# Kernel optimization log

Measured on AMD Instinct MI355X. Metric: run time of the kernel, lower is better.

## Reference

```python
import jax, jax.numpy as jnp
import numpy as np

N, E, IN, H, OUT = 50000, 600000, 256, 128, 40
EPS, GAMMA = 0.1, 0.1  # PyG AntiSymmetricConv defaults


def _build_norm(edge_index, n):
    # GCNConv normalization with added self loops: D^-1/2 (A+I) D^-1/2
    loops = jnp.arange(n, dtype=edge_index.dtype)
    src = jnp.concatenate([edge_index[0], loops])
    dst = jnp.concatenate([edge_index[1], loops])
    deg = jax.ops.segment_sum(jnp.ones(src.shape[0], dtype=jnp.float32), dst, num_segments=n)
    dinv = jnp.where(deg > 0, jax.lax.rsqrt(jnp.maximum(deg, 1e-12)), 0.0)
    return src, dst, dinv[src] * dinv[dst]


def _gcn(x, w, src, dst, norm, n):
    # GCNConv(bias=False): scatter normalized messages to target nodes
    m = (x @ w)[src] * norm[:, None]          # [E+N, d]
    return jax.ops.segment_sum(m, dst, num_segments=n)


def _antisym_conv(x, W, gcn_w, bias, src, dst, norm, num_iters):
    d = W.shape[0]
    aW = W - W.T - GAMMA * jnp.eye(d, dtype=W.dtype)  # antisymmetric weight
    n = x.shape[0]

    def step(h, _):
        upd = jnp.tanh(h @ aW.T + _gcn(h, gcn_w, src, dst, norm, n) + bias)
        return h + EPS * upd, None

    x, _ = jax.lax.scan(step, x, None, length=num_iters)
    return x


def setup_inputs() -> dict:
    key = jax.random.key(0)
    ks = jax.random.split(key, 16)
    s = lambda fan: 1.0 / np.sqrt(fan)
    return {
        "x": jax.random.normal(ks[0], (N, IN), dtype=jnp.float32),
        "edge_index": jax.random.randint(ks[1], (2, E), 0, N, dtype=jnp.int64),
        "w_hid": jax.random.normal(ks[2], (H, IN), dtype=jnp.float32) * s(IN),
        "b_hid": jax.random.normal(ks[3], (H,), dtype=jnp.float32) * s(IN),
        "W_a1": jax.random.normal(ks[4], (H, H), dtype=jnp.float32) * s(H),
        "gcn_w1": jax.random.normal(ks[5], (H, H), dtype=jnp.float32) * s(H),
        "b_a1": jax.random.normal(ks[6], (H,), dtype=jnp.float32) * s(H),
        "w_hid2": jax.random.normal(ks[7], (H // 2, H), dtype=jnp.float32) * s(H),
        "b_hid2": jax.random.normal(ks[8], (H // 2,), dtype=jnp.float32) * s(H),
        "W_a2": jax.random.normal(ks[9], (H // 2, H // 2), dtype=jnp.float32) * s(H // 2),
        "gcn_w2": jax.random.normal(ks[10], (H // 2, H // 2), dtype=jnp.float32) * s(H // 2),
        "b_a2": jax.random.normal(ks[11], (H // 2,), dtype=jnp.float32) * s(H // 2),
        "w_fc": jax.random.normal(ks[12], (OUT, H // 2), dtype=jnp.float32) * s(H // 2),
        "b_fc": jax.random.normal(ks[13], (OUT,), dtype=jnp.float32) * s(H // 2),
    }


def reference(x, edge_index, w_hid, b_hid, W_a1, gcn_w1, b_a1,
              w_hid2, b_hid2, W_a2, gcn_w2, b_a2, w_fc, b_fc):
    n = x.shape[0]
    src, dst, norm = _build_norm(edge_index, n)
    h = jax.nn.leaky_relu(x @ w_hid.T + b_hid)          # dropout is no-op in eval
    h = _antisym_conv(h, W_a1, gcn_w1, b_a1, src, dst, norm, num_iters=3)
    h = jax.nn.leaky_relu(h)
    h = jax.nn.leaky_relu(h @ w_hid2.T + b_hid2)
    h = _antisym_conv(h, W_a2, gcn_w2, b_a2, src, dst, norm, num_iters=1)
    out = h @ w_fc.T + b_fc
    return jax.nn.log_softmax(out, axis=1)
```

## Files before the change

### kernel.cpp

```cpp
#include <hip/hip_runtime.h>
#include <hip/hip_bf16.h>
#include <math.h>

typedef unsigned short u16;
typedef unsigned int   u32;
using short8  = __attribute__((ext_vector_type(8))) short;
using f32x4   = __attribute__((ext_vector_type(4))) float;

static constexpr int NNODE = 50000;
static constexpr int NEDGE = 600000;
static constexpr float EPSC   = 0.1f;
static constexpr float GAMMAC = 0.1f;

static constexpr int NTILE = (NNODE + 63) / 64;
static constexpr int GH    = 128;
static constexpr int NRNG  = 12500;
static constexpr int NWORD = NRNG / 2;
static constexpr int NPASS = 4;

static constexpr long long O_DINV   = 0;
static constexpr long long O_DEGI   = 50000;
static constexpr long long O_ROWPTR = 100000;
static constexpr long long O_GCUR   = 150004;
static constexpr long long O_ECSR   = 200260;
static constexpr long long O_WHB    = 1400260;
static constexpr long long O_G1TB   = O_WHB  + 16384;
static constexpr long long O_AW1B   = O_G1TB + 8192;
static constexpr long long O_W2B    = O_AW1B + 8192;
static constexpr long long O_AW2B   = O_W2B  + 4096;
static constexpr long long O_G2TB   = O_AW2B + 2048;
static constexpr long long O_WFCB   = O_G2TB + 2048;
static constexpr long long O_AGGB   = 3450004;
static constexpr long long O_HB0    = O_AGGB + 3200000;
static constexpr long long O_HB1    = O_HB0  + 3200000;
static constexpr long long O_S0     = O_HB1  + 3200000;
static constexpr long long O_S1     = O_S0   + 1600000;
static constexpr long long O_PART   = O_S1   + 1600000;
static constexpr long long O_BASE   = O_PART + 3200000;

__device__ __forceinline__ float bf2f(u16 u) {
    return __uint_as_float(((unsigned)u) << 16);
}
__device__ __forceinline__ u16 f2bf(float f) {
    unsigned u = __float_as_uint(f);
    return (u16)((u + 0x7FFFu + ((u >> 16) & 1u)) >> 16);
}
__device__ __forceinline__ float ftanh(float x) {
    float x2 = fminf(fmaxf(2.f * x, -30.f), 30.f);
    float e = __expf(x2);
    return (e - 1.f) * __builtin_amdgcn_rcpf(e + 1.f);
}
__device__ __forceinline__ u16 pk_fp8(float a, float b) {
    int pk = __builtin_amdgcn_cvt_pk_fp8_f32(a, b, 0, false);
    return (u16)(pk & 0xffff);
}
__device__ __forceinline__ void acc_fp8x4(float* a, u32 v, float w) {
    a[0] += __builtin_amdgcn_cvt_f32_fp8(v, 0) * w;
    a[1] += __builtin_amdgcn_cvt_f32_fp8(v, 1) * w;
    a[2] += __builtin_amdgcn_cvt_f32_fp8(v, 2) * w;
    a[3] += __builtin_amdgcn_cvt_f32_fp8(v, 3) * w;
}

__global__ __launch_bounds__(256) void prep_kernel(
    const float* __restrict__ w_hid, const float* __restrict__ W_a1,
    const float* __restrict__ gcn1,  const float* __restrict__ w2,
    const float* __restrict__ W_a2,  const float* __restrict__ gcn2,
    const float* __restrict__ wfc,   float* __restrict__ ws)
{
    int j = blockIdx.x * 256 + threadIdx.x;
    if (j < 32768) { ((u16*)(ws+O_WHB))[j] = f2bf(w_hid[j]); return; } j -= 32768;
    if (j < 16384) { int r=j>>7, c=j&127; ((u16*)(ws+O_G1TB))[j] = f2bf(gcn1[c*128+r]); return; } j -= 16384;
    if (j < 16384) { int r=j>>7, c=j&127;
                     ((u16*)(ws+O_AW1B))[j] = f2bf(W_a1[r*128+c] - W_a1[c*128+r] - (r==c?GAMMAC:0.f));
                     return; } j -= 16384;
    if (j < 8192)  { ((u16*)(ws+O_W2B))[j] = f2bf(w2[j]); return; } j -= 8192;
    if (j < 4096)  { int r=j>>6, c=j&63;
                     ((u16*)(ws+O_AW2B))[j] = f2bf(W_a2[r*64+c] - W_a2[c*64+r] - (r==c?GAMMAC:0.f));
                     return; } j -= 4096;
    if (j < 4096)  { int r=j>>6, c=j&63; ((u16*)(ws+O_G2TB))[j] = f2bf(gcn2[c*64+r]); return; } j -= 4096;
    if (j < 2560)  { ((u16*)(ws+O_WFCB))[j] = f2bf(wfc[j]); return; } j -= 2560;
    if (j == 0)    { ((int*)(ws+O_GCUR))[0] = 0; }
}

__global__ __launch_bounds__(256) void alloc_kernel(
    const u16* __restrict__ part, float* __restrict__ dinv,
    int* __restrict__ degi, int* __restrict__ rowptr,
    u16* __restrict__ base16, int* __restrict__ gcur)
{
    int i = blockIdx.x * 256 + threadIdx.x;
    int lane = threadIdx.x & 63;
    bool ok = i < NNODE;
    int deg = 0;
    if (ok) {
        int run = 0;
        #pragma unroll 4
        for (int g = 0; g < GH; ++g) {
            base16[(long long)g * NNODE + i] = (u16)run;
            run += part[(long long)g * NNODE + i];
        }
        deg = run;
        degi[i] = deg;
        dinv[i] = rsqrtf(1.0f + (float)deg);
    }
    int run = deg;
    #pragma unroll
    for (int off = 1; off < 64; off <<= 1) {
        int v = __shfl_up(run, off);
        if (lane >= off) run += v;
    }
    int tot = __shfl(run, 63);
    int basep = 0;
    if (lane == 63) basep = atomicAdd(gcur, tot);
    basep = __shfl(basep, 63);
    if (ok) rowptr[i] = basep + run - deg;
}

__global__ __launch_bounds__(256) void fill_kernel(
    const int* __restrict__ ei, const float* __restrict__ dinv,
    const int* __restrict__ rowptr, const u16* __restrict__ base16,
    int2* __restrict__ ecsr)
{
    __shared__ u32 cur[NWORD];
    const int g    = blockIdx.x >> 2;
    const int pass = blockIdx.x & 3;
    const long long e0 = (long long)g * NEDGE / GH;
    const long long e1 = (long long)(g + 1) * NEDGE / GH;
    const u16* bb = base16 + (long long)g * NNODE;
    const int nbase = pass * NRNG;
    for (int wi = threadIdx.x; wi < NWORD; wi += 256) cur[wi] = 0;
    __syncthreads();
    for (long long e = e0 + threadIdx.x; e < e1; e += 256) {
        int d = ei[NEDGE + e];
        int r = d - nbase;
        if ((unsigned)r < (unsigned)NRNG) {
            int s = ei[e];
            u32 old = atomicAdd(&cur[r >> 1], 1u << ((r & 1) * 16));
            int rank = (int)((old >> ((r & 1) * 16)) & 0xffffu);
            int slot = rowptr[d] + (int)bb[d] + rank;
            int2 v;
            v.x = s;
            v.y = __float_as_int(dinv[s]);
            ecsr[slot] = v;
        }
    }
}

template<int KS, int NT, int AF32, int LOADACT, int EPI>
__global__ __launch_bounds__(256, 4) void mgemm(
    const void* __restrict__ Araw,
    const u16* __restrict__ Bt,
    const float* __restrict__ bias,
    float* __restrict__ outF,
    u16* __restrict__ outB,
    u16* __restrict__ outB8,
    int M, int Nn, int ldc,
    const int* __restrict__ ei,
    u16* __restrict__ partial)
{
    constexpr int K    = KS * 32;
    constexpr int KCHU = (K > 128) ? 128 : K;
    constexpr int KC   = KCHU / 32;
    constexpr int NCH  = K / KCHU;
    constexpr int P    = KCHU + 8;
    constexpr int ROWS = NT * 16;
    constexpr int CW   = NT * 16 + 1;
    constexpr int BSZ  = ROWS * P * 2;
    constexpr int ASZ  = 64 * CW * 4;
    constexpr int SMEM = BSZ > ASZ ? BSZ : ASZ;
    __shared__ __align__(16) char smem[SMEM];

    if (ei && blockIdx.x >= NTILE) {
        int g = blockIdx.x - NTILE;
        u32* hist = (u32*)smem;
        const long long e0 = (long long)g * NEDGE / GH;
        const long long e1 = (long long)(g + 1) * NEDGE / GH;
        u16* part = partial + (long long)g * NNODE;
        for (int pass = 0; pass < NPASS; ++pass) {
            const int nbase = pass * NRNG;
            for (int wi = threadIdx.x; wi < NWORD; wi += 256) hist[wi] = 0;
            __syncthreads();
            for (long long e = e0 + threadIdx.x; e < e1; e += 256) {
                int d = ei[NEDGE + e];
                int r = d - nbase;
                if ((unsigned)r < (unsigned)NRNG)
                    atomicAdd(&hist[r >> 1], 1u << ((r & 1) * 16));
            }
            __syncthreads();
            for (int wi = threadIdx.x; wi < NWORD; wi += 256)
                *(u32*)&part[nbase + wi * 2] = hist[wi];
            __syncthreads();
        }
        return;
    }

    u16*   bl   = (u16*)smem;
    float* accL = (float*)smem;

    const int wave = threadIdx.x >> 6;
    const int lane = threadIdx.x & 63;
    const int m = lane & 15, q = lane >> 4;
    const int rowbase = blockIdx.x * 64 + wave * 16;
    const int row = rowbase + m;
    const bool rok = row < M;
    const short8 z8 = {0,0,0,0,0,0,0,0};

    short8 af[KS];
    if (AF32) {
        const float* apf = (const float*)Araw + (long long)row * K;
        #pragma unroll
        for (int k = 0; k < KS; ++k) {
            short8 t = z8;
            if (rok) {
                const float4* p = (const float4*)(apf + (k * 4 + q) * 8);
                float4 a = p[0], b = p[1];
                t[0]=(short)f2bf(a.x); t[1]=(short)f2bf(a.y); t[2]=(short)f2bf(a.z); t[3]=(short)f2bf(a.w);
                t[4]=(short)f2bf(b.x); t[5]=(short)f2bf(b.y); t[6]=(short)f2bf(b.z); t[7]=(short)f2bf(b.w);
            }
            af[k] = t;
        }
    } else {
        const short8* ap = (const short8*)((const u16*)Araw + (long long)row * K);
        #pragma unroll
        for (int k = 0; k < KS; ++k) af[k] = rok ? ap[k * 4 + q] : z8;
    }
    if (LOADACT) {
        #pragma unroll
        for (int k = 0; k < KS; ++k)
            #pragma unroll
            for (int e = 0; e < 8; ++e) {
                float f = bf2f((u16)af[k][e]);
                f = f > 0.f ? f : 0.01f * f;
                af[k][e] = (short)f2bf(f);
            }
    }

    f32x4 acc[NT];
    #pragma unroll
    for (int j = 0; j < NT; ++j) acc[j] = (f32x4){0.f,0.f,0.f,0.f};

    for (int ch = 0; ch < NCH; ++ch) {
        if (ch) __syncthreads();
        constexpr int CHUNKS = ROWS * (KCHU / 8);
        for (int t = threadIdx.x; t < CHUNKS; t += 256) {
            int r = t / (KCHU / 8), c = t - r * (KCHU / 8);
            short8 v = z8;
            if (r < Nn) v = *(const short8*)&Bt[(long long)r * K + ch * KCHU + c * 8];
            *(short8*)&bl[r * P + c * 8] = v;
        }
        __syncthreads();
        #pragma unroll
        for (int j = 0; j < NT; ++j) {
            #pragma unroll
            for (int k = 0; k < KC; ++k) {
                short8 bf_ = *(const short8*)&bl[(j * 16 + m) * P + k * 32 + q * 8];
                acc[j] = __builtin_amdgcn_mfma_f32_16x16x32_bf16(af[ch * KC + k], bf_, acc[j], 0, 0, 0);
            }
        }
    }

    __syncthreads();
    #pragma unroll
    for (int j = 0; j < NT; ++j)
        #pragma unroll
        for (int r = 0; r < 4; ++r)
            accL[(wave * 16 + q * 4 + r) * CW + j * 16 + m] = acc[j][r];
    __syncthreads();

    const int c0 = lane * 2;
    if (c0 < NT * 16) {
        float2 bv = {0.f, 0.f};
        if (bias) {
            if (c0 < Nn)     bv.x = bias[c0];
            if (c0 + 1 < Nn) bv.y = bias[c0 + 1];
        }
        #pragma unroll
        for (int rl = 0; rl < 16; ++rl) {
            int rowD = rowbase + rl;
            if (rowD >= M) continue;
            float2 v = *(const float2*)&accL[(wave * 16 + rl) * CW + c0];
            long long o = (long long)rowD * ldc + c0;
            v.x += bv.x; v.y += bv.y;
            if (EPI == 1) {
                v.x = v.x > 0.f ? v.x : 0.01f * v.x;
                v.y = v.y > 0.f ? v.y : 0.01f * v.y;
            }
            if (c0 + 1 < Nn) {
                if (outB) { ushort2 ob; ob.x = f2bf(v.x); ob.y = f2bf(v.y);
                            *(ushort2*)&outB[o] = ob; }
                if (outB8) outB8[o >> 1] = pk_fp8(v.x, v.y);
                if (outF) { *(float2*)&outF[o] = v; }
            } else if (c0 < Nn) {
                if (outB) outB[o] = f2bf(v.x);
                if (outF) outF[o] = v.x;
            }
        }
    }
}

template<int HD>
__global__ __launch_bounds__(256) void gather_kernel(
    const int* __restrict__ rowptr, const int* __restrict__ degi,
    const int2* __restrict__ ecsr, const float* __restrict__ dinv,
    const u32* __restrict__ g8, u16* __restrict__ aggB)
{
    int node = (blockIdx.x * 256 + threadIdx.x) >> 6;
    int lane = threadIdx.x & 63;
    if (node >= NNODE) return;
    const int qr = lane >> 4, l4 = lane & 15;
    const int r0 = rowptr[node];
    const int r1 = r0 + degi[node];
    const float dn = dinv[node];
    constexpr int EL = (HD == 128) ? 8 : 4;

    float a[EL];
    #pragma unroll
    for (int i = 0; i < EL; ++i) a[i] = 0.f;
    if (qr == 0) {
        if (HD == 128) {
            uint2 gv = ((const uint2*)g8)[(long long)node * 16 + l4];
            acc_fp8x4(a, gv.x, dn);
            acc_fp8x4(a + 4, gv.y, dn);
        } else {
            u32 gv = g8[(long long)node * 16 + l4];
            acc_fp8x4(a, gv, dn);
        }
    }

    for (int base = r0; base < r1; base += 64) {
        int idx = base + lane;
        int cs = 0; float cw = 0.f;
        if (idx < r1) { int2 ev = ecsr[idx]; cs = ev.x; cw = __int_as_float(ev.y); }
        int cnt = min(64, r1 - base);
        for (int j = 0; j < cnt; j += 16) {
            #pragma unroll
            for (int u = 0; u < 4; ++u) {
                int jj = j + u * 4 + qr;
                int   s = __shfl(cs, jj);
                float w = __shfl(cw, jj);
                if (HD == 128) {
                    uint2 gv = ((const uint2*)g8)[(long long)s * 16 + l4];
                    acc_fp8x4(a, gv.x, w);
                    acc_fp8x4(a + 4, gv.y, w);
                } else {
                    u32 gv = g8[(long long)s * 16 + l4];
                    acc_fp8x4(a, gv, w);
                }
            }
        }
    }

    #pragma unroll
    for (int i = 0; i < EL; ++i) {
        a[i] += __shfl_xor(a[i], 16);
        a[i] += __shfl_xor(a[i], 32);
    }
    if (HD == 128) {
        float v0 = (qr == 0) ? a[0] : (qr == 1) ? a[2] : (qr == 2) ? a[4] : a[6];
        float v1 = (qr == 0) ? a[1] : (qr == 1) ? a[3] : (qr == 2) ? a[5] : a[7];
        v0 *= dn; v1 *= dn;
        long long o = (long long)node * 128 + l4 * 8 + qr * 2;
        ushort2 ob; ob.x = f2bf(v0); ob.y = f2bf(v1);
        *(ushort2*)&aggB[o] = ob;
    } else {
        float v = (qr == 0) ? a[0] : (qr == 1) ? a[1] : (qr == 2) ? a[2] : a[3];
        aggB[(long long)node * 64 + l4 * 4 + qr] = f2bf(v * dn);
    }
}

template<int KS, int NT, int TAIL>
__global__ __launch_bounds__(256, TAIL ? 3 : 4) void mgemm_conv(
    const u16* __restrict__ hA,
    const u16* __restrict__ gA,
    const u16* __restrict__ BtW,
    const u16* __restrict__ BtG,
    const float* __restrict__ bias,
    u16* __restrict__ outB,
    u16* __restrict__ outB8,
    const u16* __restrict__ w2W,
    const float* __restrict__ b2,
    int M)
{
    constexpr int K    = KS * 32;
    constexpr int Nn   = NT * 16;
    constexpr int P    = K + 8;
    constexpr int CW   = Nn + 1;
    constexpr int BSZ  = Nn * P * 2;
    constexpr int ASZ  = 64 * CW * 4;
    constexpr int R1   = BSZ > ASZ ? BSZ : ASZ;
    constexpr int EXTRA = TAIL ? 64 * P * 2 : 0;
    __shared__ __align__(16) char smem[R1 + EXTRA];
    u16*   bl   = (u16*)smem;
    float* accL = (float*)smem;
    u16*   aggT = (u16*)(smem + R1);

    const int wave = threadIdx.x >> 6;
    const int lane = threadIdx.x & 63;
    const int m = lane & 15, q = lane >> 4;
    const int rowbase = blockIdx.x * 64 + wave * 16;
    const int row = rowbase + m;
    const bool rok = row < M;
    const short8 z8 = {0,0,0,0,0,0,0,0};

    short8 af1[KS], af2[KS];
    {
        const short8* ap1 = (const short8*)(hA + (long long)row * K);
        const short8* ap2 = (const short8*)(gA + (long long)row * K);
        #pragma unroll
        for (int k = 0; k < KS; ++k) {
            af1[k] = rok ? ap1[k * 4 + q] : z8;
            af2[k] = rok ? ap2[k * 4 + q] : z8;
        }
    }

    f32x4 acc[NT];
    #pragma unroll
    for (int j = 0; j < NT; ++j) acc[j] = (f32x4){0.f,0.f,0.f,0.f};

    #pragma unroll
    for (int pass = 0; pass < 2; ++pass) {
        const u16* Bcur = pass ? BtG : BtW;
        if (pass) __syncthreads();
        constexpr int CHUNKS = Nn * (K / 8);
        for (int t = threadIdx.x; t < CHUNKS; t += 256) {
            int r = t / (K / 8), c = t - r * (K / 8);
            *(short8*)&bl[r * P + c * 8] = *(const short8*)&Bcur[(long long)r * K + c * 8];
        }
        __syncthreads();
        #pragma unroll
        for (int j = 0; j < NT; ++j) {
            #pragma unroll
            for (int k = 0; k < KS; ++k) {
                short8 bf_ = *(const short8*)&bl[(j * 16 + m) * P + k * 32 + q * 8];
                acc[j] = __builtin_amdgcn_mfma_f32_16x16x32_bf16(
                    pass ? af2[k] : af1[k], bf_, acc[j], 0, 0, 0);
            }
        }
    }

    __syncthreads();
    #pragma unroll
    for (int j = 0; j < NT; ++j)
        #pragma unroll
        for (int r = 0; r < 4; ++r)
            accL[(wave * 16 + q * 4 + r) * CW + j * 16 + m] = acc[j][r];
    __syncthreads();

    const int c0 = lane * 2;
    if (TAIL == 0) {
        if (c0 < Nn) {
            float2 bv = {bias[c0], bias[c0 + 1]};
            #pragma unroll
            for (int rl = 0; rl < 16; ++rl) {
                int rowD = rowbase + rl;
                if (rowD >= M) continue;
                float2 v = *(const float2*)&accL[(wave * 16 + rl) * CW + c0];
                long long o = (long long)rowD * Nn + c0;
                ushort2 hh = *(const ushort2*)&hA[o];
                float n0 = bf2f(hh.x) + EPSC * ftanh(v.x + bv.x);
                float n1 = bf2f(hh.y) + EPSC * ftanh(v.y + bv.y);
                ushort2 ob; ob.x = f2bf(n0); ob.y = f2bf(n1);
                *(ushort2*)&outB[o] = ob;
                if (outB8) outB8[o >> 1] = pk_fp8(n0, n1);
            }
        }
        return;
    }

    {
        float2 bv = {bias[c0], bias[c0 + 1]};
        #pragma unroll
        for (int rl = 0; rl < 16; ++rl) {
            int rowD = rowbase + rl;
            float n0 = 0.f, n1 = 0.f;
            if (rowD < M) {
                float2 v = *(const float2*)&accL[(wave * 16 + rl) * CW + c0];
                long long o = (long long)rowD * K + c0;
                ushort2 hh = *(const ushort2*)&hA[o];
                n0 = bf2f(hh.x) + EPSC * ftanh(v.x + bv.x);
                n1 = bf2f(hh.y) + EPSC * ftanh(v.y + bv.y);
                n0 = n0 > 0.f ? n0 : 0.01f * n0;
                n1 = n1 > 0.f ? n1 : 0.01f * n1;
            }
            ushort2 ob; ob.x = f2bf(n0); ob.y = f2bf(n1);
            *(ushort2*)&aggT[(wave * 16 + rl) * P + c0] = ob;
        }
    }
    __syncthreads();

    short8 af3[4];
    #pragma unroll
    for (int k = 0; k < 4; ++k)
        af3[k] = *(const short8*)&aggT[(wave * 16 + m) * P + k * 32 + q * 8];

    {
        constexpr int CH2 = 64 * 16;
        for (int t = threadIdx.x; t < CH2; t += 256) {
            int r = t >> 4, c = t & 15;
            *(short8*)&bl[r * P + c * 8] = *(const short8*)&w2W[(long long)r * K + c * 8];
        }
    }
    __syncthreads();

    f32x4 acc2[4];
    #pragma unroll
    for (int j = 0; j < 4; ++j) acc2[j] = (f32x4){0.f,0.f,0.f,0.f};
    #pragma unroll
    for (int j = 0; j < 4; ++j)
        #pragma unroll
        for (int k = 0; k < 4; ++k) {
            short8 bf_ = *(const short8*)&bl[(j * 16 + m) * P + k * 32 + q * 8];
            acc2[j] = __builtin_amdgcn_mfma_f32_16x16x32_bf16(af3[k], bf_, acc2[j], 0, 0, 0);
        }

    __syncthreads();
    constexpr int CW2 = 65;
    #pragma unroll
    for (int j = 0; j < 4; ++j)
        #pragma unroll
        for (int r = 0; r < 4; ++r)
            accL[(wave * 16 + q * 4 + r) * CW2 + j * 16 + m] = acc2[j][r];
    __syncthreads();

    if (c0 < 64) {
        float2 bv = {b2[c0], b2[c0 + 1]};
        #pragma unroll
        for (int rl = 0; rl < 16; ++rl) {
            int rowD = rowbase + rl;
            if (rowD >= M) continue;
            float2 v = *(const float2*)&accL[(wave * 16 + rl) * CW2 + c0];
            v.x += bv.x; v.y += bv.y;
            v.x = v.x > 0.f ? v.x : 0.01f * v.x;
            v.y = v.y > 0.f ? v.y : 0.01f * v.y;
            long long o = (long long)rowD * 64 + c0;
            ushort2 ob; ob.x = f2bf(v.x); ob.y = f2bf(v.y);
            *(ushort2*)&outB[o] = ob;
            outB8[o >> 1] = pk_fp8(v.x, v.y);
        }
    }
}

__global__ __launch_bounds__(256, 4) void conv2fc(
    const u16* __restrict__ hA,
    const u16* __restrict__ gA,
    const u16* __restrict__ BtW, const u16* __restrict__ BtG,
    const float* __restrict__ bias,
    const u16* __restrict__ wfcB, const float* __restrict__ bfc,
    float* __restrict__ outF, int M)
{
    constexpr int K  = 64, NT = 4, KS = 2;
    constexpr int P  = K + 8;
    constexpr int CW = 65;
    constexpr int R1 = 64 * CW * 4;
    __shared__ __align__(16) char smem[R1 + 64 * P * 2];
    u16*   bl   = (u16*)smem;
    float* accL = (float*)smem;
    u16*   aggT = (u16*)(smem + R1);

    const int wave = threadIdx.x >> 6;
    const int lane = threadIdx.x & 63;
    const int m = lane & 15, q = lane >> 4;
    const int rowbase = blockIdx.x * 64 + wave * 16;
    const int row = rowbase + m;
    const bool rok = row < M;
    const short8 z8 = {0,0,0,0,0,0,0,0};

    short8 af1[KS], af2[KS];
    {
        const short8* ap1 = (const short8*)(hA + (long long)row * K);
        const short8* ap2 = (const short8*)(gA + (long long)row * K);
        #pragma unroll
        for (int k = 0; k < KS; ++k) {
            af1[k] = rok ? ap1[k * 4 + q] : z8;
            af2[k] = rok ? ap2[k * 4 + q] : z8;
        }
    }

    f32x4 acc[NT];
    #pragma unroll
    for (int j = 0; j < NT; ++j) acc[j] = (f32x4){0.f,0.f,0.f,0.f};

    #pragma unroll
    for (int pass = 0; pass < 2; ++pass) {
        const u16* Bcur = pass ? BtG : BtW;
        if (pass) __syncthreads();
        constexpr int CHUNKS = 64 * (K / 8);
        for (int t = threadIdx.x; t < CHUNKS; t += 256) {
            int r = t >> 3, c = t & 7;
            *(short8*)&bl[r * P + c * 8] = *(const short8*)&Bcur[(long long)r * K + c * 8];
        }
        __syncthreads();
        #pragma unroll
        for (int j = 0; j < NT; ++j)
            #pragma unroll
            for (int k = 0; k < KS; ++k) {
                short8 bf_ = *(const short8*)&bl[(j * 16 + m) * P + k * 32 + q * 8];
                acc[j] = __builtin_amdgcn_mfma_f32_16x16x32_bf16(
                    pass ? af2[k] : af1[k], bf_, acc[j], 0, 0, 0);
            }
    }

    __syncthreads();
    #pragma unroll
    for (int j = 0; j < NT; ++j)
        #pragma unroll
        for (int r = 0; r < 4; ++r)
            accL[(wave * 16 + q * 4 + r) * CW + j * 16 + m] = acc[j][r];
    __syncthreads();

    {
        const int c0 = lane * 2;
        float2 bv = {bias[c0 & 63], bias[(c0 + 1) & 63]};
        if (c0 < 64) {
            #pragma unroll
            for (int rl = 0; rl < 16; ++rl) {
                int rowD = rowbase + rl;
                float n0 = 0.f, n1 = 0.f;
                if (rowD < M) {
                    float2 v = *(const float2*)&accL[(wave * 16 + rl) * CW + c0];
                    long long o = (long long)rowD * 64 + c0;
                    ushort2 hh = *(const ushort2*)&hA[o];
                    n0 = bf2f(hh.x) + EPSC * ftanh(v.x + bv.x);
                    n1 = bf2f(hh.y) + EPSC * ftanh(v.y + bv.y);
                }
                ushort2 ob; ob.x = f2bf(n0); ob.y = f2bf(n1);
                *(ushort2*)&aggT[(wave * 16 + rl) * P + c0] = ob;
            }
        }
    }
    __syncthreads();

    short8 af4[KS];
    #pragma unroll
    for (int k = 0; k < KS; ++k)
        af4[k] = *(const short8*)&aggT[(wave * 16 + m) * P + k * 32 + q * 8];

    {
        constexpr int CHF = 48 * 8;
        for (int t = threadIdx.x; t < CHF; t += 256) {
            int r = t >> 3, c = t & 7;
            short8 v = z8;
            if (r < 40) v = *(const short8*)&wfcB[(long long)r * K + c * 8];
            *(short8*)&bl[r * P + c * 8] = v;
        }
    }
    __syncthreads();

    f32x4 acc3[3];
    #pragma unroll
    for (int j = 0; j < 3; ++j) acc3[j] = (f32x4){0.f,0.f,0.f,0.f};
    #pragma unroll
    for (int j = 0; j < 3; ++j)
        #pragma unroll
        for (int k = 0; k < KS; ++k) {
            short8 bf_ = *(const short8*)&bl[(j * 16 + m) * P + k * 32 + q * 8];
            acc3[j] = __builtin_amdgcn_mfma_f32_16x16x32_bf16(af4[k], bf_, acc3[j], 0, 0, 0);
        }

    __syncthreads();
    constexpr int CW3 = 49;
    #pragma unroll
    for (int j = 0; j < 3; ++j)
        #pragma unroll
        for (int r = 0; r < 4; ++r)
            accL[(wave * 16 + q * 4 + r) * CW3 + j * 16 + m] = acc3[j][r];
    __syncthreads();

    float mrow = 0.f, lrow = 0.f;
    if (lane < 16) {
        const float* rp = &accL[(wave * 16 + lane) * CW3];
        float mx = -1e30f;
        for (int c = 0; c < 40; ++c) mx = fmaxf(mx, rp[c] + bfc[c]);
        float s = 0.f;
        for (int c = 0; c < 40; ++c) s += expf(rp[c] + bfc[c] - mx);
        mrow = mx; lrow = logf(s);
    }
    for (int rl = 0; rl < 16; ++rl) {
        float mm = __shfl(mrow, rl);
        float ll = __shfl(lrow, rl);
        int rowD = rowbase + rl;
        if (rowD < M && lane < 40) {
            float v = accL[(wave * 16 + rl) * CW3 + lane] + bfc[lane];
            outF[(long long)rowD * 40 + lane] = v - mm - ll;
        }
    }
}

extern "C" void kernel_launch(void* const* d_in, const int* in_sizes, int n_in,
                              void* d_out, int out_size, void* d_ws, size_t ws_size,
                              hipStream_t stream) {
    const float* x     = (const float*)d_in[0];
    const int*   ei    = (const int*)d_in[1];
    const float* w_hid = (const float*)d_in[2];
    const float* b_hid = (const float*)d_in[3];
    const float* W_a1  = (const float*)d_in[4];
    const float* gcn1  = (const float*)d_in[5];
    const float* b_a1  = (const float*)d_in[6];
    const float* w2    = (const float*)d_in[7];
    const float* b2    = (const float*)d_in[8];
    const float* W_a2  = (const float*)d_in[9];
    const float* gcn2  = (const float*)d_in[10];
    const float* b_a2  = (const float*)d_in[11];
    const float* wfc   = (const float*)d_in[12];
    const float* bfc   = (const float*)d_in[13];
    float* ws = (float*)d_ws;
    float* out = (float*)d_out;

    float* dinv   = ws + O_DINV;
    int*   degi   = (int*)(ws + O_DEGI);
    int*   rowptr = (int*)(ws + O_ROWPTR);
    int*   gcur   = (int*)(ws + O_GCUR);
    int2*  ecsr   = (int2*)(ws + O_ECSR);
    u16* whB  = (u16*)(ws + O_WHB);
    u16* g1tB = (u16*)(ws + O_G1TB);
    u16* aw1B = (u16*)(ws + O_AW1B);
    u16* w2B  = (u16*)(ws + O_W2B);
    u16* aw2B = (u16*)(ws + O_AW2B);
    u16* g2tB = (u16*)(ws + O_G2TB);
    u16* wfcB = (u16*)(ws + O_WFCB);
    u16* aggB = (u16*)(ws + O_AGGB);
    u16* hB0  = (u16*)(ws + O_HB0);
    u16* hB1  = (u16*)(ws + O_HB1);
    u16* s0   = (u16*)(ws + O_S0);
    u16* s1   = (u16*)(ws + O_S1);
    u16* part = (u16*)(ws + O_PART);
    u16* base16 = (u16*)(ws + O_BASE);

    prep_kernel<<<(84481 + 255) / 256, 256, 0, stream>>>(
        w_hid, W_a1, gcn1, w2, W_a2, gcn2, wfc, ws);

    const int gatherBlocks = (NNODE * 64 + 255) / 256;

    mgemm<8, 8, 1, 0, 1><<<NTILE + GH, 256, 0, stream>>>(
        x, whB, b_hid, nullptr, hB0, s0, NNODE, 128, 128, ei, part);

    alloc_kernel<<<(NNODE + 255) / 256, 256, 0, stream>>>(
        part, dinv, degi, rowptr, base16, gcur);
    fill_kernel<<<GH * NPASS, 256, 0, stream>>>(ei, dinv, rowptr, base16, ecsr);

    gather_kernel<128><<<gatherBlocks, 256, 0, stream>>>(
        rowptr, degi, ecsr, dinv, (const u32*)s0, aggB);
    mgemm_conv<4, 8, 0><<<NTILE, 256, 0, stream>>>(
        hB0, aggB, aw1B, g1tB, b_a1, hB1, s1, nullptr, nullptr, NNODE);
    gather_kernel<128><<<gatherBlocks, 256, 0, stream>>>(
        rowptr, degi, ecsr, dinv, (const u32*)s1, aggB);
    mgemm_conv<4, 8, 0><<<NTILE, 256, 0, stream>>>(
        hB1, aggB, aw1B, g1tB, b_a1, hB0, s0, nullptr, nullptr, NNODE);
    gather_kernel<128><<<gatherBlocks, 256, 0, stream>>>(
        rowptr, degi, ecsr, dinv, (const u32*)s0, aggB);
    mgemm_conv<4, 8, 1><<<NTILE, 256, 0, stream>>>(
        hB0, aggB, aw1B, g1tB, b_a1, hB1, s1, w2B, b2, NNODE);

    gather_kernel<64><<<gatherBlocks, 256, 0, stream>>>(
        rowptr, degi, ecsr, dinv, (const u32*)s1, aggB);
    conv2fc<<<NTILE, 256, 0, stream>>>(
        hB1, aggB, aw2B, g2tB, b_a2, wfcB, bfc, out, NNODE);
}
```

Before: 362.9 us.

## Fuse first-iteration gather into conv GEMM and shrink tail conv shared memory

Adds an fconv kernel, 512 threads per block, that gathers the fp8 neighbour features for 64 nodes into shared memory and then runs both conv GEMMs and the tanh update in the same block. It replaces the first gather_kernel plus mgemm_conv pair, so the aggregated tensor no longer makes a round trip through global memory and one launch is removed. The tail variant of mgemm_conv now reuses its main shared buffer for the aggregate tile and the second weight, staging values in registers across a barrier so it can run with launch bounds of 4 instead of 3. The risk is that the gather phase in fconv uses fewer, larger blocks, which may give less latency hiding than the standalone gather.

New measurement: 355.9 us. No clear change (-1.9%).

```diff
diff --git a/kernel.cpp b/kernel.cpp
--- a/kernel.cpp
+++ b/kernel.cpp
@@ -367,8 +367,136 @@
     }
 }
 
+__global__ __launch_bounds__(512, 3) void fconv(
+    const u16* __restrict__ hA, const u32* __restrict__ g8,
+    const int* __restrict__ rowptr, const int* __restrict__ degi,
+    const int2* __restrict__ ecsr, const float* __restrict__ dinv,
+    const u16* __restrict__ BtW, const u16* __restrict__ BtG,
+    const float* __restrict__ bias,
+    u16* __restrict__ outB, u16* __restrict__ outB8)
+{
+    constexpr int K = 128, P = 136;
+    __shared__ __align__(16) char smem[52224];
+    u16* bl   = (u16*)smem;
+    u16* aggT = (u16*)(smem + 34816);
+    const int wave = threadIdx.x >> 6, lane = threadIdx.x & 63;
+    const int m = lane & 15, q = lane >> 4;
+    const int blockrow = blockIdx.x * 64;
+    const short8 z8 = {0,0,0,0,0,0,0,0};
+
+    {
+        const int qr = q, l4 = m;
+        for (int nn = 0; nn < 8; ++nn) {
+            int lr = wave * 8 + nn;
+            int node = blockrow + lr;
+            if (node >= NNODE) break;
+            const int r0 = rowptr[node];
+            const int r1 = r0 + degi[node];
+            const float dn = dinv[node];
+            float a[8] = {0.f,0.f,0.f,0.f,0.f,0.f,0.f,0.f};
+            if (qr == 0) {
+                uint2 gv = ((const uint2*)g8)[(long long)node * 16 + l4];
+                acc_fp8x4(a, gv.x, dn);
+                acc_fp8x4(a + 4, gv.y, dn);
+            }
+            for (int base = r0; base < r1; base += 64) {
+                int idx = base + lane;
+                int cs = 0; float cw = 0.f;
+                if (idx < r1) { int2 ev = ecsr[idx]; cs = ev.x; cw = __int_as_float(ev.y); }
+                int cnt = min(64, r1 - base);
+                for (int j = 0; j < cnt; j += 16) {
+                    #pragma unroll
+                    for (int u = 0; u < 4; ++u) {
+                        int jj = j + u * 4 + qr;
+                        int   s = __shfl(cs, jj);
+                        float w = __shfl(cw, jj);
+                        uint2 gv = ((const uint2*)g8)[(long long)s * 16 + l4];
+                        acc_fp8x4(a, gv.x, w);
+                        acc_fp8x4(a + 4, gv.y, w);
+                    }
+                }
+            }
+            #pragma unroll
+            for (int i = 0; i < 8; ++i) {
+                a[i] += __shfl_xor(a[i], 16);
+                a[i] += __shfl_xor(a[i], 32);
+            }
+            float v0 = (qr == 0) ? a[0] : (qr == 1) ? a[2] : (qr == 2) ? a[4] : a[6];
+            float v1 = (qr == 0) ? a[1] : (qr == 1) ? a[3] : (qr == 2) ? a[5] : a[7];
+            v0 *= dn; v1 *= dn;
+            ushort2 ob; ob.x = f2bf(v0); ob.y = f2bf(v1);
+            *(ushort2*)&aggT[lr * P + l4 * 8 + qr * 2] = ob;
+        }
+    }
+    __syncthreads();
+
+    const int nh = wave >> 2;
+    const int rowbase = blockrow + (wave & 3) * 16;
+    const int row = rowbase + m;
+    const bool rok = row < NNODE;
+
+    short8 af1[4], af2[4];
+    {
+        const short8* ap1 = (const short8*)(hA + (long long)row * K);
+        #pragma unroll
+        for (int k = 0; k < 4; ++k) {
+            af1[k] = rok ? ap1[k * 4 + q] : z8;
+            af2[k] = rok ? *(const short8*)&aggT[((wave & 3) * 16 + m) * P + k * 32 + q * 8] : z8;
+        }
+    }
+
+    f32x4 acc[4];
+    #pragma unroll
+    for (int j = 0; j < 4; ++j) acc[j] = (f32x4){0.f,0.f,0.f,0.f};
+
+    #pragma unroll
+    for (int pass = 0; pass < 2; ++pass) {
+        const u16* Bsrc = pass ? BtG : BtW;
+        if (pass) __syncthreads();
+        for (int t = threadIdx.x; t < 2048; t += 512) {
+            int r = t >> 4, c = t & 15;
+            *(short8*)&bl[r * P + c * 8] = *(const short8*)&Bsrc[(long long)r * K + c * 8];
+        }
+        __syncthreads();
+        #pragma unroll
+        for (int j = 0; j < 4; ++j)
+            #pragma unroll
+            for (int kk = 0; kk < 4; ++kk) {
+                short8 b_ = *(const short8*)&bl[(nh*64 + j*16 + m) * P + kk*32 + q*8];
+                acc[j] = __builtin_amdgcn_mfma_f32_16x16x32_bf16(
+                    pass ? af2[kk] : af1[kk], b_, acc[j], 0, 0, 0);
+            }
+    }
+
+    __syncthreads();
+    float* accW = (float*)smem + wave * 16 * 65;
+    #pragma unroll
+    for (int j = 0; j < 4; ++j)
+        #pragma unroll
+        for (int r = 0; r < 4; ++r)
+            accW[(q*4 + r) * 65 + j*16 + m] = acc[j][r];
+
+    const int hw = lane >> 5;
+    const int c0 = (lane & 31) * 2;
+    float2 bv = {bias[nh*64 + c0], bias[nh*64 + c0 + 1]};
+    #pragma unroll
+    for (int rl8 = 0; rl8 < 8; ++rl8) {
+        int rl = hw * 8 + rl8;
+        int rowD = rowbase + rl;
+        if (rowD >= NNODE) continue;
+        float2 v = *(const float2*)&accW[rl * 65 + c0];
+        long long o = (long long)rowD * 128 + nh*64 + c0;
+        ushort2 hh = *(const ushort2*)&hA[o];
+        float n0 = bf2f(hh.x) + EPSC * ftanh(v.x + bv.x);
+        float n1 = bf2f(hh.y) + EPSC * ftanh(v.y + bv.y);
+        ushort2 ob; ob.x = f2bf(n0); ob.y = f2bf(n1);
+        *(ushort2*)&outB[o] = ob;
+        outB8[o >> 1] = pk_fp8(n0, n1);
+    }
+}
+
 template<int KS, int NT, int TAIL>
-__global__ __launch_bounds__(256, TAIL ? 3 : 4) void mgemm_conv(
+__global__ __launch_bounds__(256, 4) void mgemm_conv(
     const u16* __restrict__ hA,
     const u16* __restrict__ gA,
     const u16* __restrict__ BtW,
@@ -387,11 +515,9 @@
     constexpr int BSZ  = Nn * P * 2;
     constexpr int ASZ  = 64 * CW * 4;
     constexpr int R1   = BSZ > ASZ ? BSZ : ASZ;
-    constexpr int EXTRA = TAIL ? 64 * P * 2 : 0;
-    __shared__ __align__(16) char smem[R1 + EXTRA];
+    __shared__ __align__(16) char smem[R1];
     u16*   bl   = (u16*)smem;
     float* accL = (float*)smem;
-    u16*   aggT = (u16*)(smem + R1);
 
     const int wave = threadIdx.x >> 6;
     const int lane = threadIdx.x & 63;
@@ -466,6 +592,7 @@
         return;
     }
 
+    u32 hv[16];
     {
         float2 bv = {bias[c0], bias[c0 + 1]};
         #pragma unroll
@@ -481,9 +608,19 @@
                 n0 = n0 > 0.f ? n0 : 0.01f * n0;
                 n1 = n1 > 0.f ? n1 : 0.01f * n1;
             }
-            ushort2 ob; ob.x = f2bf(n0); ob.y = f2bf(n1);
-            *(ushort2*)&aggT[(wave * 16 + rl) * P + c0] = ob;
-        }
+            hv[rl] = (u32)f2bf(n0) | ((u32)f2bf(n1) << 16);
+        }
+    }
+    __syncthreads();
+
+    u16* aggT = (u16*)smem;
+    u16* bl2  = (u16*)(smem + 17408);
+    #pragma unroll
+    for (int rl = 0; rl < 16; ++rl)
+        *(u32*)&aggT[(wave * 16 + rl) * P + c0] = hv[rl];
+    for (int t = threadIdx.x; t < 1024; t += 256) {
+        int r = t >> 4, c = t & 15;
+        *(short8*)&bl2[r * P + c * 8] = *(const short8*)&w2W[(long long)r * K + c * 8];
     }
     __syncthreads();
 
@@ -492,15 +629,6 @@
     for (int k = 0; k < 4; ++k)
         af3[k] = *(const short8*)&aggT[(wave * 16 + m) * P + k * 32 + q * 8];
 
-    {
-        constexpr int CH2 = 64 * 16;
-        for (int t = threadIdx.x; t < CH2; t += 256) {
-            int r = t >> 4, c = t & 15;
-            *(short8*)&bl[r * P + c * 8] = *(const short8*)&w2W[(long long)r * K + c * 8];
-        }
-    }
-    __syncthreads();
-
     f32x4 acc2[4];
     #pragma unroll
     for (int j = 0; j < 4; ++j) acc2[j] = (f32x4){0.f,0.f,0.f,0.f};
@@ -508,17 +636,18 @@
     for (int j = 0; j < 4; ++j)
         #pragma unroll
         for (int k = 0; k < 4; ++k) {
-            short8 bf_ = *(const short8*)&bl[(j * 16 + m) * P + k * 32 + q * 8];
+            short8 bf_ = *(const short8*)&bl2[(j * 16 + m) * P + k * 32 + q * 8];
             acc2[j] = __builtin_amdgcn_mfma_f32_16x16x32_bf16(af3[k], bf_, acc2[j], 0, 0, 0);
         }
 
     __syncthreads();
     constexpr int CW2 = 65;
+    float* accL2 = (float*)smem;
     #pragma unroll
     for (int j = 0; j < 4; ++j)
         #pragma unroll
         for (int r = 0; r < 4; ++r)
-            accL[(wave * 16 + q * 4 + r) * CW2 + j * 16 + m] = acc2[j][r];
+            accL2[(wave * 16 + q * 4 + r) * CW2 + j * 16 + m] = acc2[j][r];
     __syncthreads();
 
     if (c0 < 64) {
@@ -527,7 +656,7 @@
         for (int rl = 0; rl < 16; ++rl) {
             int rowD = rowbase + rl;
             if (rowD >= M) continue;
-            float2 v = *(const float2*)&accL[(wave * 16 + rl) * CW2 + c0];
+            float2 v = *(const float2*)&accL2[(wave * 16 + rl) * CW2 + c0];
             v.x += bv.x; v.y += bv.y;
             v.x = v.x > 0.f ? v.x : 0.01f * v.x;
             v.y = v.y > 0.f ? v.y : 0.01f * v.y;
@@ -737,10 +866,8 @@
         part, dinv, degi, rowptr, base16, gcur);
     fill_kernel<<<GH * NPASS, 256, 0, stream>>>(ei, dinv, rowptr, base16, ecsr);
 
-    gather_kernel<128><<<gatherBlocks, 256, 0, stream>>>(
-        rowptr, degi, ecsr, dinv, (const u32*)s0, aggB);
-    mgemm_conv<4, 8, 0><<<NTILE, 256, 0, stream>>>(
-        hB0, aggB, aw1B, g1tB, b_a1, hB1, s1, nullptr, nullptr, NNODE);
+    fconv<<<NTILE, 512, 0, stream>>>(hB0, (const u32*)s0, rowptr, degi, ecsr, dinv,
+                                     aw1B, g1tB, b_a1, hB1, s1);
     gather_kernel<128><<<gatherBlocks, 256, 0, stream>>>(
         rowptr, degi, ecsr, dinv, (const u32*)s1, aggB);
     mgemm_conv<4, 8, 0><<<NTILE, 256, 0, stream>>>(
```
